# Kernel optimization log

Hardware: AMD Instinct MI355X
Metric: run time of the kernel (lower is better)

The kernel has to match this reference:

```python
import jax, jax.numpy as jnp
import numpy as np

BN_EPS = 1e-5


def conv2d(x, w, b, pad=1):
    # x: [B,Ci,H,W], w: [Co,Ci,kh,kw] (torch OIHW layout)
    y = jax.lax.conv_general_dilated(
        x, w, window_strides=(1, 1), padding=((pad, pad), (pad, pad)),
        dimension_numbers=("NCHW", "OIHW", "NCHW"))
    return y + b[None, :, None, None]


def conv_transpose2d(x, w, b):
    # torch ConvTranspose2d(k=3, stride=2, padding=1, output_padding=1)
    # w: [Ci, Co, 3, 3] (torch transpose-conv layout)
    # equivalent: lhs-dilated conv with flipped kernel, pad = (k-1-p, k-1-p+op) = (1, 2)
    wk = jnp.flip(w, axis=(2, 3)).transpose(1, 0, 2, 3)  # [Co, Ci, 3, 3]
    y = jax.lax.conv_general_dilated(
        x, wk, window_strides=(1, 1), padding=((1, 2), (1, 2)),
        lhs_dilation=(2, 2), dimension_numbers=("NCHW", "OIHW", "NCHW"))
    return y + b[None, :, None, None]


def setup_inputs() -> dict:
    key = jax.random.key(0)
    ks = jax.random.split(key, 10)
    B, Cin, Cout, E = 1024, 128, 64, 8
    s = lambda k, shape: jax.random.normal(k, shape, jnp.float32) * 0.05
    return {
        "x": jax.random.normal(ks[0], (B, Cin, 6, 6), jnp.float32),
        # gate params
        "gw": s(ks[1], (128, Cin, 3, 3)), "gb": jnp.zeros((128,), jnp.float32),
        "fc1_w": s(ks[2], (256, 128 * 9)), "fc1_b": jnp.zeros((256,), jnp.float32),
        "fc2_w": s(ks[3], (E, 256)), "fc2_b": jnp.zeros((E,), jnp.float32),
        # expert params, stacked over expert axis E (num_per_expert=1 block)
        "wd": s(ks[4], (E, Cin, Cout, 3, 3)), "bd": jnp.zeros((E, Cout), jnp.float32),
        "wc": s(ks[5], (E, Cout, Cout, 3, 3)), "bc": jnp.zeros((E, Cout), jnp.float32),
        # BatchNorm (inference / running stats)
        "bn_g": jnp.ones((E, Cout), jnp.float32),
        "bn_b": jnp.zeros((E, Cout), jnp.float32),
        "bn_m": s(ks[6], (E, Cout)),
        "bn_v": jax.random.uniform(ks[7], (E, Cout), jnp.float32, 0.5, 1.5),
        "top_k": 2,
    }


def reference(x, gw, gb, fc1_w, fc1_b, fc2_w, fc2_b,
              wd, bd, wc, bc, bn_g, bn_b, bn_m, bn_v, top_k):
    B = x.shape[0]

    # --- Gate: conv3x3 -> relu -> maxpool2x2 -> fc -> relu -> fc ---
    h = jax.nn.relu(conv2d(x, gw, gb))                       # [B,128,6,6]
    p = jax.lax.reduce_window(h, -jnp.inf, jax.lax.max,
                              (1, 1, 2, 2), (1, 1, 2, 2), "VALID")  # [B,128,3,3]
    z = jax.nn.relu(p.reshape(B, -1) @ fc1_w.T + fc1_b)
    logits = z @ fc2_w.T + fc2_b                             # [B,E]

    # --- All experts computed densely (as in source), vmapped over expert axis ---
    def expert(wd_e, bd_e, wc_e, bc_e, g_e, b_e, m_e, v_e):
        y = jax.nn.relu(conv_transpose2d(x, wd_e, bd_e))     # [B,Cout,12,12]
        y = conv2d(y, wc_e, bc_e)
        scale = (g_e * jax.lax.rsqrt(v_e + BN_EPS))[None, :, None, None]
        y = (y - m_e[None, :, None, None]) * scale + b_e[None, :, None, None]
        return jax.nn.relu(y)

    eo = jax.vmap(expert)(wd, bd, wc, bc, bn_g, bn_b, bn_m, bn_v)  # [E,B,C,12,12]

    # --- top-k routing: gather selected experts, softmax-weighted sum ---
    tw, ti = jax.lax.top_k(logits, top_k)                    # [B,k]
    tw = jax.nn.softmax(tw, axis=1)
    sel = jnp.take_along_axis(eo.transpose(1, 0, 2, 3, 4),
                              ti[:, :, None, None, None], axis=1)  # [B,k,C,12,12]
    return (sel * tw[:, :, None, None, None]).sum(axis=1)   # [B,C,12,12]
```

## Files before the change

### kernel.cpp

```cpp
#include <hip/hip_runtime.h>
#include <math.h>

typedef _Float16 f16x8 __attribute__((ext_vector_type(8)));
typedef float    f32x4 __attribute__((ext_vector_type(4)));

#define PWD_ELEMS 589824
#define PWC_ELEMS 294912
#define PWG_ELEMS 147456
#define PW1T_ELEMS 294912
#define WS_NEEDED_BYTES ((PWD_ELEMS + PWC_ELEMS + 2 * PWG_ELEMS) * 2 + 512 * 4 + 16384 + PW1T_ELEMS * 4)

__global__ void pack_weights(const float* __restrict__ wd,
                             const float* __restrict__ wc,
                             const float* __restrict__ gw,
                             const float* __restrict__ fc1_w,
                             const float* __restrict__ bc,
                             const float* __restrict__ bn_g,
                             const float* __restrict__ bn_b,
                             const float* __restrict__ bn_m,
                             const float* __restrict__ bn_v,
                             _Float16* __restrict__ pwd,
                             _Float16* __restrict__ pwc,
                             _Float16* __restrict__ pwg_hi,
                             _Float16* __restrict__ pwg_lo,
                             float* __restrict__ pbias,
                             float* __restrict__ pw1t)
{
  int i = blockIdx.x * 256 + threadIdx.x;
  if (i < PWD_ELEMS) {
    int j  = i & 7;
    int l  = (i >> 3) & 63;
    int nt = (i >> 9) & 3;
    int ks = (i >> 11) & 3;
    int rest = i >> 13;
    int t = rest % 9, e = rest / 9;
    int ky = t / 3, kx = t % 3;
    int k = ks * 32 + (l >> 4) * 8 + j;
    int n = nt * 16 + (l & 15);
    float v = wd[(((size_t)e * 128 + k) * 64 + n) * 9 + (2 - ky) * 3 + (2 - kx)];
    pwd[i] = (_Float16)v;
    return;
  }
  i -= PWD_ELEMS;
  if (i < PWC_ELEMS) {
    int j  = i & 7;
    int l  = (i >> 3) & 63;
    int nt = (i >> 9) & 3;
    int ks = (i >> 11) & 1;
    int rest = i >> 12;
    int t = rest % 9, e = rest / 9;
    int ky = t / 3, kx = t % 3;
    int k = ks * 32 + (l >> 4) * 8 + j;
    int n = nt * 16 + (l & 15);
    float scale = bn_g[e * 64 + n] * rsqrtf(bn_v[e * 64 + n] + 1e-5f);
    float v = wc[(((size_t)e * 64 + n) * 64 + k) * 9 + ky * 3 + kx] * scale;
    pwc[i] = (_Float16)v;
    return;
  }
  i -= PWC_ELEMS;
  if (i < PWG_ELEMS) {
    int j  = i & 7;
    int l  = (i >> 3) & 63;
    int nt = (i >> 9) & 7;
    int ks = (i >> 12) & 3;
    int t  = i >> 14;
    int ky = t / 3, kx = t % 3;
    int k = ks * 32 + (l >> 4) * 8 + j;
    int n = nt * 16 + (l & 15);
    float v = gw[(size_t)n * 1152 + k * 9 + ky * 3 + kx];
    _Float16 hi = (_Float16)v;
    pwg_hi[i] = hi;
    pwg_lo[i] = (_Float16)(v - (float)hi);
    return;
  }
  i -= PWG_ELEMS;
  if (i < 512) {
    int e = i >> 6, n = i & 63;
    float scale = bn_g[e * 64 + n] * rsqrtf(bn_v[e * 64 + n] + 1e-5f);
    pbias[i] = (bc[e * 64 + n] - bn_m[e * 64 + n]) * scale + bn_b[e * 64 + n];
    return;
  }
  i -= 512;
  if (i < PW1T_ELEMS) {
    int k = i >> 8, o = i & 255;
    pw1t[i] = fc1_w[(size_t)o * 1152 + k];
  }
}

__global__ __launch_bounds__(256, 4) void cmoe_gate(
    const float* __restrict__ x, const float* __restrict__ gb,
    const float* __restrict__ pw1t, const float* __restrict__ fc1_b,
    const float* __restrict__ fc2_w, const float* __restrict__ fc2_b,
    const _Float16* __restrict__ pwg_hi, const _Float16* __restrict__ pwg_lo,
    int* __restrict__ route_i, float* __restrict__ route_w)
{
  const int b = blockIdx.x;
  const int tid = threadIdx.x;

  __shared__ __align__(16) char smem[34816];
  _Float16* xg_hi = (_Float16*)smem;
  _Float16* xg_lo = (_Float16*)(smem + 17408);
  float* hbuf = (float*)smem;
  float* pbuf = (float*)(smem + 18432);
  float* zred = (float*)(smem + 23040);
  float* zbuf = (float*)(smem + 27136);
  float* slog = (float*)(smem + 28160);

  const int w    = tid >> 6;
  const int lane = tid & 63;
  const int lr   = lane & 15;
  const int lq   = lane >> 4;

  const float* xb = x + (size_t)b * 4608;
  for (int idx = tid; idx < 8192; idx += 256) {
    int sp = idx >> 7, ci = idx & 127;
    int row = sp >> 3, col = sp & 7;
    float v = 0.f;
    if (row >= 1 && row <= 6 && col >= 1 && col <= 6)
      v = xb[ci * 36 + (row - 1) * 6 + (col - 1)];
    _Float16 hi = (_Float16)v;
    xg_hi[sp * 136 + ci] = hi;
    xg_lo[sp * 136 + ci] = (_Float16)(v - (float)hi);
  }
  __syncthreads();

  {
    f32x4 Cg[3][2];
    {
      float b0 = gb[(2 * w) * 16 + lr];
      float b1 = gb[(2 * w + 1) * 16 + lr];
#pragma unroll
      for (int i = 0; i < 3; ++i) {
        Cg[i][0] = {b0, b0, b0, b0};
        Cg[i][1] = {b1, b1, b1, b1};
      }
    }
    int gA[3];
#pragma unroll
    for (int i = 0; i < 3; ++i) {
      int p = i * 16 + lr; if (p >= 36) p = 0;
      int oy = p / 6, ox = p % 6;
      gA[i] = (oy * 8 + ox) * 136 + lq * 8;
    }
    const _Float16* pgh = pwg_hi + lane * 8;
    const _Float16* pgl = pwg_lo + lane * 8;

    for (int t = 0; t < 9; ++t) {
      const int gtap = ((t / 3) * 8 + (t % 3)) * 136;
#pragma unroll
      for (int ks = 0; ks < 4; ++ks) {
        const int boff = ((t * 4 + ks) * 8 + 2 * w) * 512;
        f16x8 Bh0 = *(const f16x8*)(pgh + boff);
        f16x8 Bh1 = *(const f16x8*)(pgh + boff + 512);
        f16x8 Bl0 = *(const f16x8*)(pgl + boff);
        f16x8 Bl1 = *(const f16x8*)(pgl + boff + 512);
#pragma unroll
        for (int i = 0; i < 3; ++i) {
          f16x8 Ah = *(const f16x8*)(xg_hi + gA[i] + gtap + ks * 32);
          f16x8 Al = *(const f16x8*)(xg_lo + gA[i] + gtap + ks * 32);
          Cg[i][0] = __builtin_amdgcn_mfma_f32_16x16x32_f16(Ah, Bh0, Cg[i][0], 0, 0, 0);
          Cg[i][1] = __builtin_amdgcn_mfma_f32_16x16x32_f16(Ah, Bh1, Cg[i][1], 0, 0, 0);
          Cg[i][0] = __builtin_amdgcn_mfma_f32_16x16x32_f16(Al, Bh0, Cg[i][0], 0, 0, 0);
          Cg[i][1] = __builtin_amdgcn_mfma_f32_16x16x32_f16(Al, Bh1, Cg[i][1], 0, 0, 0);
          Cg[i][0] = __builtin_amdgcn_mfma_f32_16x16x32_f16(Ah, Bl0, Cg[i][0], 0, 0, 0);
          Cg[i][1] = __builtin_amdgcn_mfma_f32_16x16x32_f16(Ah, Bl1, Cg[i][1], 0, 0, 0);
        }
      }
    }
    __syncthreads();
#pragma unroll
    for (int i = 0; i < 3; ++i)
#pragma unroll
      for (int nn = 0; nn < 2; ++nn) {
        const int co_ = (2 * w + nn) * 16 + lr;
#pragma unroll
        for (int j = 0; j < 4; ++j) {
          int pix = i * 16 + lq * 4 + j;
          if (pix < 36) hbuf[co_ * 36 + pix] = fmaxf(Cg[i][nn][j], 0.f);
        }
      }
  }
  __syncthreads();

  for (int i = tid; i < 1152; i += 256) {
    int co_ = i / 9, r = i % 9, py = r / 3, px = r % 3;
    const float* hp = hbuf + co_ * 36 + (2 * py) * 6 + 2 * px;
    pbuf[i] = fmaxf(fmaxf(hp[0], hp[1]), fmaxf(hp[6], hp[7]));
  }
  __syncthreads();

  {
    const int g = lane;
    const float* pw = pw1t + w * 256 + 4 * g;
    f32x4 acc = {0.f, 0.f, 0.f, 0.f};
#pragma unroll 4
    for (int m = 0; m < 288; ++m) {
      float pv = pbuf[w + 4 * m];
      f32x4 wv = *(const f32x4*)(pw + m * 1024);
      acc.x += wv.x * pv; acc.y += wv.y * pv;
      acc.z += wv.z * pv; acc.w += wv.w * pv;
    }
    *(f32x4*)&zred[w * 256 + 4 * g] = acc;
  }
  __syncthreads();
  zbuf[tid] = fmaxf(zred[tid] + zred[256 + tid] + zred[512 + tid] + zred[768 + tid]
                    + fc1_b[tid], 0.f);
  __syncthreads();

  if (tid < 64) {
    int o = tid >> 3, t8 = tid & 7;
    float acc = 0.f;
    const float* wr = fc2_w + o * 256;
    for (int k = t8; k < 256; k += 8) acc += zbuf[k] * wr[k];
    acc += __shfl_xor(acc, 1);
    acc += __shfl_xor(acc, 2);
    acc += __shfl_xor(acc, 4);
    if (t8 == 0) slog[o] = acc + fc2_b[o];
  }
  __syncthreads();

  if (tid == 0) {
    int i0 = 0; float v0 = slog[0];
#pragma unroll
    for (int o = 1; o < 8; ++o) { float v = slog[o]; if (v > v0) { v0 = v; i0 = o; } }
    int i1 = (i0 == 0) ? 1 : 0; float v1 = slog[i1];
#pragma unroll
    for (int o = 0; o < 8; ++o) {
      if (o != i0) { float v = slog[o]; if (v > v1) { v1 = v; i1 = o; } }
    }
    float e1 = expf(v1 - v0);
    float inv = 1.f / (1.f + e1);
    route_i[2 * b] = i0; route_i[2 * b + 1] = i1;
    route_w[2 * b] = inv; route_w[2 * b + 1] = e1 * inv;
  }
}

#define ZOFF  4896
#define Y1OFF 5024

#define DECONV_TAP(KY, KX)                                                  \
  {                                                                         \
    constexpr int t_  = (KY) * 3 + (KX);                                    \
    constexpr int dy_ = ((KY) == 2) ? 1 : 0;                                \
    constexpr int dx_ = ((KX) == 2) ? 1 : 0;                                \
    int u0 = uA[0] + dy_, v0 = vA[0] + dx_;                                 \
    int u1 = uA[1] + dy_, v1 = vA[1] + dx_;                                 \
    int u2 = uA[2] + dy_, v2 = vA[2] + dx_;                                 \
    int b0_ = (pvA[0] && u0 < 6 && v0 < 6) ? (u0 * 6 + v0) * 136 : ZOFF;    \
    int b1_ = (pvA[1] && u1 < 6 && v1 < 6) ? (u1 * 6 + v1) * 136 : ZOFF;    \
    int b2_ = (pvA[2] && u2 < 6 && v2 < 6) ? (u2 * 6 + v2) * 136 : ZOFF;    \
    _Pragma("unroll")                                                       \
    for (int ks = 0; ks < 4; ++ks) {                                        \
      f16x8 Bf = *(const f16x8*)(pwd_e + (size_t)(t_ * 4 + ks) * 2048);     \
      f16x8 A0 = *(const f16x8*)(S + b0_ + lq * 8 + ks * 32);               \
      f16x8 A1 = *(const f16x8*)(S + b1_ + lq * 8 + ks * 32);               \
      f16x8 A2 = *(const f16x8*)(S + b2_ + lq * 8 + ks * 32);               \
      Cd0 = __builtin_amdgcn_mfma_f32_16x16x32_f16(A0, Bf, Cd0, 0, 0, 0);   \
      Cd1 = __builtin_amdgcn_mfma_f32_16x16x32_f16(A1, Bf, Cd1, 0, 0, 0);   \
      Cd2 = __builtin_amdgcn_mfma_f32_16x16x32_f16(A2, Bf, Cd2, 0, 0, 0);   \
    }                                                                       \
  }

#define STORE_CLASS(QY, QX)                                                 \
  _Pragma("unroll")                                                         \
  for (int i = 0; i < 3; ++i) {                                             \
    f32x4 Cv = (i == 0) ? Cd0 : ((i == 1) ? Cd1 : Cd2);                     \
    _Pragma("unroll")                                                       \
    for (int j = 0; j < 4; ++j) {                                           \
      int p = i * 16 + lq * 4 + j;                                          \
      if (p < 36) {                                                         \
        int u = p / 6, v = p - 6 * (p / 6);                                 \
        int oy = 2 * u + (QY), ox = 2 * v + (QX);                           \
        S[Y1OFF + ((oy + 1) * 14 + (ox + 1)) * 72 + co] =                   \
            (_Float16)fmaxf(Cv[j], 0.f);                                    \
      }                                                                     \
    }                                                                       \
  }

__global__ __launch_bounds__(256, 4) void cmoe_expert(
    const float* __restrict__ x,
    const float* __restrict__ bd,
    const _Float16* __restrict__ pwd, const _Float16* __restrict__ pwc,
    const float* __restrict__ pbias,
    const int* __restrict__ route_i, const float* __restrict__ route_w,
    float* __restrict__ out)
{
  const int b = blockIdx.x;
  const int tid = threadIdx.x;

  __shared__ __align__(16) char smem[38272];
  _Float16* S = (_Float16*)smem;
  float* sout = (float*)(smem + 10048);

  const int w    = tid >> 6;
  const int lane = tid & 63;
  const int lr   = lane & 15;
  const int lq   = lane >> 4;

  const int e0 = route_i[2 * b], e1 = route_i[2 * b + 1];
  const float w0 = route_w[2 * b], w1 = route_w[2 * b + 1];

  const float* xb = x + (size_t)b * 4608;
  for (int idx = tid; idx < 4608; idx += 256) {
    int ci = idx / 36, pix = idx - ci * 36;
    S[pix * 136 + ci] = (_Float16)xb[idx];
  }
  if (tid < 128) S[ZOFF + tid] = (_Float16)0.f;
  for (int idx = tid; idx < 52 * 72; idx += 256) {
    int sp = idx / 72, ci = idx % 72;
    int row, col;
    if (sp < 14)      { row = 0;       col = sp; }
    else if (sp < 28) { row = 13;      col = sp - 14; }
    else if (sp < 40) { row = sp - 27; col = 0; }
    else              { row = sp - 39; col = 13; }
    S[Y1OFF + (row * 14 + col) * 72 + ci] = (_Float16)0.f;
  }

  const int co = w * 16 + lr;

  int uA[3], vA[3], pvA[3];
#pragma unroll
  for (int i = 0; i < 3; ++i) {
    int p = i * 16 + lr;
    pvA[i] = (p < 36);
    int pc = pvA[i] ? p : 0;
    uA[i] = pc / 6; vA[i] = pc - 6 * (pc / 6);
  }
  int cA[9];
#pragma unroll
  for (int mt = 0; mt < 9; ++mt) {
    int pix = mt * 16 + lr;
    int oy = pix / 12, ox = pix - 12 * (pix / 12);
    cA[mt] = Y1OFF + (oy * 14 + ox) * 72 + lq * 8;
  }

  f32x4 facc[9];
#pragma unroll
  for (int mt = 0; mt < 9; ++mt) facc[mt] = {0.f, 0.f, 0.f, 0.f};

#pragma unroll 1
  for (int s = 0; s < 2; ++s) {
    const int e = s ? e1 : e0;
    const float wgt = s ? w1 : w0;
    const float db = bd[e * 64 + co];
    const _Float16* pwd_e = pwd + (size_t)e * (9 * 4 * 4 * 512) + w * 512 + lane * 8;

    __syncthreads();

    {
      f32x4 Cd0 = {db, db, db, db}, Cd1 = Cd0, Cd2 = Cd0;
      DECONV_TAP(0, 0) DECONV_TAP(0, 2) DECONV_TAP(2, 0) DECONV_TAP(2, 2)
      STORE_CLASS(1, 1)
    }
    {
      f32x4 Cd0 = {db, db, db, db}, Cd1 = Cd0, Cd2 = Cd0;
      DECONV_TAP(0, 1) DECONV_TAP(2, 1)
      STORE_CLASS(1, 0)
    }
    {
      f32x4 Cd0 = {db, db, db, db}, Cd1 = Cd0, Cd2 = Cd0;
      DECONV_TAP(1, 0) DECONV_TAP(1, 2)
      STORE_CLASS(0, 1)
    }
    {
      f32x4 Cd0 = {db, db, db, db}, Cd1 = Cd0, Cd2 = Cd0;
      DECONV_TAP(1, 1)
      STORE_CLASS(0, 0)
    }
    __syncthreads();

    f32x4 Cc[9];
    {
      const float cb = pbias[e * 64 + co];
#pragma unroll
      for (int mt = 0; mt < 9; ++mt) Cc[mt] = {cb, cb, cb, cb};
    }
    const _Float16* pwc_e = pwc + (size_t)e * (9 * 2 * 4 * 512) + w * 512 + lane * 8;

#pragma unroll
    for (int t = 0; t < 9; ++t) {
      const int ky = t / 3, kx = t % 3;
      const int aoff = (ky * 14 + kx) * 72;
#pragma unroll
      for (int ks = 0; ks < 2; ++ks) {
        f16x8 Bf = *(const f16x8*)(pwc_e + (size_t)(t * 2 + ks) * 2048);
#pragma unroll
        for (int mt = 0; mt < 9; ++mt) {
          f16x8 Af = *(const f16x8*)(S + cA[mt] + aoff + ks * 32);
          Cc[mt] = __builtin_amdgcn_mfma_f32_16x16x32_f16(Af, Bf, Cc[mt], 0, 0, 0);
        }
      }
    }

#pragma unroll
    for (int mt = 0; mt < 9; ++mt)
#pragma unroll
      for (int j = 0; j < 4; ++j)
        facc[mt][j] += wgt * fmaxf(Cc[mt][j], 0.f);
  }

  float* ob = out + (size_t)b * 9216;
  __syncthreads();
#pragma unroll
  for (int mt = 0; mt < 9; ++mt)
#pragma unroll
    for (int j = 0; j < 4; ++j) {
      int pix = mt * 16 + lq * 4 + j;
      if (pix < 72) sout[pix * 65 + co] = facc[mt][j];
    }
  __syncthreads();
  for (int j2 = tid; j2 < 4608; j2 += 256) {
    int c2 = j2 / 72, px = j2 - 72 * c2;
    ob[c2 * 144 + px] = sout[px * 65 + c2];
  }
  __syncthreads();
#pragma unroll
  for (int mt = 0; mt < 9; ++mt)
#pragma unroll
    for (int j = 0; j < 4; ++j) {
      int pix = mt * 16 + lq * 4 + j;
      if (pix >= 72) sout[(pix - 72) * 65 + co] = facc[mt][j];
    }
  __syncthreads();
  for (int j2 = tid; j2 < 4608; j2 += 256) {
    int c2 = j2 / 72, px = j2 - 72 * c2;
    ob[c2 * 144 + 72 + px] = sout[px * 65 + c2];
  }
}


#define DECONV_TAPS(q, ky, r)                                              \
  _Pragma("unroll")                                                        \
  for (int ox = 0; ox < 12; ++ox) {                                        \
    _Pragma("unroll")                                                      \
    for (int kx = 0; kx < 3; ++kx) {                                       \
      const int ss = ox + kx - 1;                                          \
      if (ss >= 0 && ss <= 10 && (ss & 1) == 0)                            \
        dacc[q][ox] += xr[r][ss >> 1] * w9[8 - ((ky) * 3 + (kx))];         \
    }                                                                      \
  }

__global__ __launch_bounds__(256, 2) void cmoe_ref(
    const float* __restrict__ x,
    const float* __restrict__ gw, const float* __restrict__ gb,
    const float* __restrict__ fc1_w, const float* __restrict__ fc1_b,
    const float* __restrict__ fc2_w, const float* __restrict__ fc2_b,
    const float* __restrict__ wd, const float* __restrict__ bd,
    const float* __restrict__ wc, const float* __restrict__ bc,
    const float* __restrict__ bn_g, const float* __restrict__ bn_b,
    const float* __restrict__ bn_m, const float* __restrict__ bn_v,
    float* __restrict__ out)
{
  const int b = blockIdx.x;
  const int tid = threadIdx.x;

  __shared__ float sx[128 * 48];
  __shared__ float sbuf[64 * 168];
  __shared__ int   se[2];
  __shared__ float swv[2];

  const float* xb = x + (size_t)b * 4608;
  for (int i = tid; i < 4608; i += 256) {
    int ci = i / 36, rem = i % 36;
    sx[ci * 48 + 6 + rem] = xb[i];
  }
  for (int i = tid; i < 128 * 12; i += 256) {
    int ci = i / 12, j = i % 12;
    sx[ci * 48 + (j < 6 ? j : 36 + j)] = 0.f;
  }
  __syncthreads();

  {
    const int co = tid >> 1;
    const int hh = tid & 1;
    float hacc[3][6];
    const float bias = gb[co];
#pragma unroll
    for (int q = 0; q < 3; ++q)
#pragma unroll
      for (int ox = 0; ox < 6; ++ox) hacc[q][ox] = bias;

    const float* wbase = gw + co * 1152;
    const float* xsb = sx + hh * 18;
    for (int ci = 0; ci < 128; ++ci) {
      const float* wr = wbase + ci * 9;
      float w9[9];
#pragma unroll
      for (int k = 0; k < 9; ++k) w9[k] = wr[k];
      const float* xr = xsb + ci * 48;
#pragma unroll
      for (int s = 0; s < 5; ++s) {
        float r8[8];
        r8[0] = 0.f; r8[7] = 0.f;
#pragma unroll
        for (int c = 0; c < 6; ++c) r8[c + 1] = xr[s * 6 + c];
#pragma unroll
        for (int ky = 0; ky < 3; ++ky) {
          const int q = s - ky;
          if (q >= 0 && q < 3) {
#pragma unroll
            for (int ox = 0; ox < 6; ++ox)
#pragma unroll
              for (int kx = 0; kx < 3; ++kx)
                hacc[q][ox] += r8[ox + kx] * w9[ky * 3 + kx];
          }
        }
      }
    }
#pragma unroll
    for (int q = 0; q < 3; ++q)
#pragma unroll
      for (int ox = 0; ox < 6; ++ox)
        sbuf[co * 36 + (3 * hh + q) * 6 + ox] = fmaxf(hacc[q][ox], 0.f);
  }
  __syncthreads();

  {
    float* sp = sbuf + 4608;
    for (int i = tid; i < 1152; i += 256) {
      int co = i / 9, r = i % 9, py = r / 3, px = r % 3;
      const float* hp = sbuf + co * 36 + (2 * py) * 6 + 2 * px;
      sp[i] = fmaxf(fmaxf(hp[0], hp[1]), fmaxf(hp[6], hp[7]));
    }
  }
  __syncthreads();

  {
    const float* sp = sbuf + 4608;
    float* sz = sbuf + 5760;
    float acc = fc1_b[tid];
    const float4* wr = (const float4*)(fc1_w + (size_t)tid * 1152);
    const float4* p4 = (const float4*)sp;
#pragma unroll 4
    for (int k = 0; k < 288; ++k) {
      float4 wv4 = wr[k], pv = p4[k];
      acc += wv4.x * pv.x + wv4.y * pv.y + wv4.z * pv.z + wv4.w * pv.w;
    }
    sz[tid] = fmaxf(acc, 0.f);
  }
  __syncthreads();

  {
    const float* sz = sbuf + 5760;
    float* slog = sbuf + 6016;
    if (tid < 8) {
      float acc = fc2_b[tid];
      const float* wr = fc2_w + tid * 256;
      for (int k = 0; k < 256; ++k) acc += sz[k] * wr[k];
      slog[tid] = acc;
    }
  }
  __syncthreads();

  if (tid == 0) {
    const float* slog = sbuf + 6016;
    int i0 = 0; float v0 = slog[0];
#pragma unroll
    for (int o = 1; o < 8; ++o) { float v = slog[o]; if (v > v0) { v0 = v; i0 = o; } }
    int i1 = (i0 == 0) ? 1 : 0; float v1 = slog[i1];
#pragma unroll
    for (int o = 0; o < 8; ++o) {
      if (o != i0) { float v = slog[o]; if (v > v1) { v1 = v; i1 = o; } }
    }
    float e1 = expf(v1 - v0);
    float inv = 1.f / (1.f + e1);
    se[0] = i0; se[1] = i1; swv[0] = inv; swv[1] = e1 * inv;
  }
  __syncthreads();

  for (int i = tid; i < 64 * 24; i += 256) {
    int ci = i / 24, j = i % 24;
    sbuf[ci * 168 + (j < 12 ? j : 144 + j)] = 0.f;
  }

  const int wv = tid >> 6;
  const int co = tid & 63;
  const int iyb = (wv & 1) ? (3 * wv - 1) / 2 : (3 * wv) / 2;

  float facc[3][12];
#pragma unroll
  for (int q = 0; q < 3; ++q)
#pragma unroll
    for (int ox = 0; ox < 12; ++ox) facc[q][ox] = 0.f;

  for (int slot = 0; slot < 2; ++slot) {
    const int e = se[slot];
    const float wgt = swv[slot];

    float dacc[3][12];
    {
      const float db = bd[e * 64 + co];
#pragma unroll
      for (int q = 0; q < 3; ++q)
#pragma unroll
        for (int ox = 0; ox < 12; ++ox) dacc[q][ox] = db;

      const float* wdb = wd + ((size_t)e * 128 * 64 + co) * 9;
      for (int ci = 0; ci < 128; ++ci) {
        const float* wr = wdb + (size_t)ci * 576;
        float w9[9];
#pragma unroll
        for (int k = 0; k < 9; ++k) w9[k] = wr[k];
        float xr[3][6];
#pragma unroll
        for (int r = 0; r < 3; ++r)
#pragma unroll
          for (int c = 0; c < 6; ++c)
            xr[r][c] = sx[ci * 48 + (iyb + r + 1) * 6 + c];
        if (wv & 1) {
          DECONV_TAPS(0, 0, 0)
          DECONV_TAPS(0, 2, 1)
          DECONV_TAPS(1, 1, 1)
          DECONV_TAPS(2, 0, 1)
          DECONV_TAPS(2, 2, 2)
        } else {
          DECONV_TAPS(0, 1, 0)
          DECONV_TAPS(1, 0, 0)
          DECONV_TAPS(1, 2, 1)
          DECONV_TAPS(2, 1, 1)
        }
      }
    }

    __syncthreads();
#pragma unroll
    for (int q = 0; q < 3; ++q)
#pragma unroll
      for (int ox = 0; ox < 12; ++ox)
        sbuf[co * 168 + (3 * wv + q + 1) * 12 + ox] = fmaxf(dacc[q][ox], 0.f);
    __syncthreads();

    float cacc[3][12];
    const float cb = bc[e * 64 + co];
#pragma unroll
    for (int q = 0; q < 3; ++q)
#pragma unroll
      for (int ox = 0; ox < 12; ++ox) cacc[q][ox] = cb;

    const float* wcb = wc + ((size_t)e * 64 + co) * 576;
    for (int ci = 0; ci < 64; ++ci) {
      const float* wr = wcb + ci * 9;
      float w9[9];
#pragma unroll
      for (int k = 0; k < 9; ++k) w9[k] = wr[k];
#pragma unroll
      for (int s = 0; s < 5; ++s) {
        float r14[14];
        r14[0] = 0.f; r14[13] = 0.f;
#pragma unroll
        for (int c = 0; c < 12; ++c) r14[c + 1] = sbuf[ci * 168 + (3 * wv + s) * 12 + c];
#pragma unroll
        for (int ky = 0; ky < 3; ++ky) {
          const int q = s - ky;
          if (q >= 0 && q < 3) {
#pragma unroll
            for (int ox = 0; ox < 12; ++ox)
#pragma unroll
              for (int kx = 0; kx < 3; ++kx)
                cacc[q][ox] += r14[ox + kx] * w9[ky * 3 + kx];
          }
        }
      }
    }

    const float g = bn_g[e * 64 + co], bb = bn_b[e * 64 + co];
    const float mm = bn_m[e * 64 + co], vvv = bn_v[e * 64 + co];
    const float scale = g * rsqrtf(vvv + 1e-5f);
#pragma unroll
    for (int q = 0; q < 3; ++q)
#pragma unroll
      for (int ox = 0; ox < 12; ++ox) {
        float v = (cacc[q][ox] - mm) * scale + bb;
        facc[q][ox] += wgt * fmaxf(v, 0.f);
      }
  }

  float* ob = out + ((size_t)b * 64 + co) * 144;
#pragma unroll
  for (int q = 0; q < 3; ++q)
#pragma unroll
    for (int ox = 0; ox < 12; ++ox)
      ob[(3 * wv + q) * 12 + ox] = facc[q][ox];
}

extern "C" void kernel_launch(void* const* d_in, const int* in_sizes, int n_in,
                              void* d_out, int out_size, void* d_ws, size_t ws_size,
                              hipStream_t stream) {
  const float* x     = (const float*)d_in[0];
  const float* gw    = (const float*)d_in[1];
  const float* gb    = (const float*)d_in[2];
  const float* fc1_w = (const float*)d_in[3];
  const float* fc1_b = (const float*)d_in[4];
  const float* fc2_w = (const float*)d_in[5];
  const float* fc2_b = (const float*)d_in[6];
  const float* wd    = (const float*)d_in[7];
  const float* bd    = (const float*)d_in[8];
  const float* wc    = (const float*)d_in[9];
  const float* bc    = (const float*)d_in[10];
  const float* bn_g  = (const float*)d_in[11];
  const float* bn_b  = (const float*)d_in[12];
  const float* bn_m  = (const float*)d_in[13];
  const float* bn_v  = (const float*)d_in[14];
  float* out = (float*)d_out;

  if (ws_size >= (size_t)WS_NEEDED_BYTES && d_ws != nullptr) {
    _Float16* pwd    = (_Float16*)d_ws;
    _Float16* pwc    = pwd + PWD_ELEMS;
    _Float16* pwg_hi = pwc + PWC_ELEMS;
    _Float16* pwg_lo = pwg_hi + PWG_ELEMS;
    float*    pbias  = (float*)(pwg_lo + PWG_ELEMS);
    int*      route_i = (int*)(pbias + 512);
    float*    route_w = (float*)(route_i + 2048);
    float*    pw1t   = route_w + 2048;

    int total = PWD_ELEMS + PWC_ELEMS + PWG_ELEMS + 512 + PW1T_ELEMS;
    pack_weights<<<dim3((total + 255) / 256), dim3(256), 0, stream>>>(
        wd, wc, gw, fc1_w, bc, bn_g, bn_b, bn_m, bn_v,
        pwd, pwc, pwg_hi, pwg_lo, pbias, pw1t);
    cmoe_gate<<<dim3(1024), dim3(256), 0, stream>>>(
        x, gb, pw1t, fc1_b, fc2_w, fc2_b, pwg_hi, pwg_lo, route_i, route_w);
    cmoe_expert<<<dim3(1024), dim3(256), 0, stream>>>(
        x, bd, pwd, pwc, pbias, route_i, route_w, out);
  } else {
    cmoe_ref<<<dim3(1024), dim3(256), 0, stream>>>(
        x, gw, gb, fc1_w, fc1_b, fc2_w, fc2_b,
        wd, bd, wc, bc, bn_g, bn_b, bn_m, bn_v, out);
  }
}
```

Before: 170.7 us.

## Process two samples per gate block to reuse conv and fc1 weight loads

The gate kernel now handles two batch samples per workgroup: it stages both inputs in shared memory, reuses each loaded gate-conv weight fragment for MFMAs on both samples, and reuses each fc1 weight vector for two dot products. The grid is halved and shared memory roughly doubles, with launch bounds relaxed to 2 blocks per CU. This targets the global/L2 weight traffic of the gate, at the cost of lower occupancy and fewer blocks in flight.

```diff
diff --git a/kernel.cpp b/kernel.cpp
--- a/kernel.cpp
+++ b/kernel.cpp
@@ -87,60 +87,61 @@
   }
 }
 
-__global__ __launch_bounds__(256, 4) void cmoe_gate(
+__global__ __launch_bounds__(256, 2) void cmoe_gate(
     const float* __restrict__ x, const float* __restrict__ gb,
     const float* __restrict__ pw1t, const float* __restrict__ fc1_b,
     const float* __restrict__ fc2_w, const float* __restrict__ fc2_b,
     const _Float16* __restrict__ pwg_hi, const _Float16* __restrict__ pwg_lo,
     int* __restrict__ route_i, float* __restrict__ route_w)
 {
-  const int b = blockIdx.x;
+  const int b2 = blockIdx.x;
   const int tid = threadIdx.x;
 
-  __shared__ __align__(16) char smem[34816];
+  __shared__ __align__(16) char smem[72256];
   _Float16* xg_hi = (_Float16*)smem;
-  _Float16* xg_lo = (_Float16*)(smem + 17408);
-  float* hbuf = (float*)smem;
-  float* pbuf = (float*)(smem + 18432);
-  float* zred = (float*)(smem + 23040);
-  float* zbuf = (float*)(smem + 27136);
-  float* slog = (float*)(smem + 28160);
+  _Float16* xg_lo = (_Float16*)(smem + 34816);
+  float* zred = (float*)(smem + 44032);
+  float* slog = (float*)(smem + 54272);
 
   const int w    = tid >> 6;
   const int lane = tid & 63;
   const int lr   = lane & 15;
   const int lq   = lane >> 4;
 
-  const float* xb = x + (size_t)b * 4608;
-  for (int idx = tid; idx < 8192; idx += 256) {
-    int sp = idx >> 7, ci = idx & 127;
+  for (int idx = tid; idx < 2 * 8192; idx += 256) {
+    int s  = idx >> 13;
+    int r  = idx & 8191;
+    int sp = r >> 7, ci = r & 127;
     int row = sp >> 3, col = sp & 7;
     float v = 0.f;
     if (row >= 1 && row <= 6 && col >= 1 && col <= 6)
-      v = xb[ci * 36 + (row - 1) * 6 + (col - 1)];
+      v = x[(size_t)(2 * b2 + s) * 4608 + ci * 36 + (row - 1) * 6 + (col - 1)];
     _Float16 hi = (_Float16)v;
-    xg_hi[sp * 136 + ci] = hi;
-    xg_lo[sp * 136 + ci] = (_Float16)(v - (float)hi);
-  }
-  __syncthreads();
+    xg_hi[s * 8704 + sp * 136 + ci] = hi;
+    xg_lo[s * 8704 + sp * 136 + ci] = (_Float16)(v - (float)hi);
+  }
+  __syncthreads();
+
+  int gA[3];
+#pragma unroll
+  for (int i = 0; i < 3; ++i) {
+    int p = i * 16 + lr; if (p >= 36) p = 0;
+    int oy = p / 6, ox = p % 6;
+    gA[i] = (oy * 8 + ox) * 136 + lq * 8;
+  }
 
   {
-    f32x4 Cg[3][2];
+    f32x4 Cg[2][3][2];
     {
       float b0 = gb[(2 * w) * 16 + lr];
       float b1 = gb[(2 * w + 1) * 16 + lr];
 #pragma unroll
-      for (int i = 0; i < 3; ++i) {
-        Cg[i][0] = {b0, b0, b0, b0};
-        Cg[i][1] = {b1, b1, b1, b1};
-      }
-    }
-    int gA[3];
-#pragma unroll
-    for (int i = 0; i < 3; ++i) {
-      int p = i * 16 + lr; if (p >= 36) p = 0;
-      int oy = p / 6, ox = p % 6;
-      gA[i] = (oy * 8 + ox) * 136 + lq * 8;
+      for (int s = 0; s < 2; ++s)
+#pragma unroll
+        for (int i = 0; i < 3; ++i) {
+          Cg[s][i][0] = {b0, b0, b0, b0};
+          Cg[s][i][1] = {b1, b1, b1, b1};
+        }
     }
     const _Float16* pgh = pwg_hi + lane * 8;
     const _Float16* pgl = pwg_lo + lane * 8;
@@ -155,83 +156,124 @@
         f16x8 Bl0 = *(const f16x8*)(pgl + boff);
         f16x8 Bl1 = *(const f16x8*)(pgl + boff + 512);
 #pragma unroll
-        for (int i = 0; i < 3; ++i) {
-          f16x8 Ah = *(const f16x8*)(xg_hi + gA[i] + gtap + ks * 32);
-          f16x8 Al = *(const f16x8*)(xg_lo + gA[i] + gtap + ks * 32);
-          Cg[i][0] = __builtin_amdgcn_mfma_f32_16x16x32_f16(Ah, Bh0, Cg[i][0], 0, 0, 0);
-          Cg[i][1] = __builtin_amdgcn_mfma_f32_16x16x32_f16(Ah, Bh1, Cg[i][1], 0, 0, 0);
-          Cg[i][0] = __builtin_amdgcn_mfma_f32_16x16x32_f16(Al, Bh0, Cg[i][0], 0, 0, 0);
-          Cg[i][1] = __builtin_amdgcn_mfma_f32_16x16x32_f16(Al, Bh1, Cg[i][1], 0, 0, 0);
-          Cg[i][0] = __builtin_amdgcn_mfma_f32_16x16x32_f16(Ah, Bl0, Cg[i][0], 0, 0, 0);
-          Cg[i][1] = __builtin_amdgcn_mfma_f32_16x16x32_f16(Ah, Bl1, Cg[i][1], 0, 0, 0);
+        for (int s = 0; s < 2; ++s)
+#pragma unroll
+          for (int i = 0; i < 3; ++i) {
+            f16x8 Ah = *(const f16x8*)(xg_hi + s * 8704 + gA[i] + gtap + ks * 32);
+            f16x8 Al = *(const f16x8*)(xg_lo + s * 8704 + gA[i] + gtap + ks * 32);
+            Cg[s][i][0] = __builtin_amdgcn_mfma_f32_16x16x32_f16(Ah, Bh0, Cg[s][i][0], 0, 0, 0);
+            Cg[s][i][1] = __builtin_amdgcn_mfma_f32_16x16x32_f16(Ah, Bh1, Cg[s][i][1], 0, 0, 0);
+            Cg[s][i][0] = __builtin_amdgcn_mfma_f32_16x16x32_f16(Al, Bh0, Cg[s][i][0], 0, 0, 0);
+            Cg[s][i][1] = __builtin_amdgcn_mfma_f32_16x16x32_f16(Al, Bh1, Cg[s][i][1], 0, 0, 0);
+            Cg[s][i][0] = __builtin_amdgcn_mfma_f32_16x16x32_f16(Ah, Bl0, Cg[s][i][0], 0, 0, 0);
+            Cg[s][i][1] = __builtin_amdgcn_mfma_f32_16x16x32_f16(Ah, Bl1, Cg[s][i][1], 0, 0, 0);
+          }
+      }
+    }
+    __syncthreads();
+#pragma unroll
+    for (int s = 0; s < 2; ++s) {
+      float* hb = (float*)(smem + 34816 + s * 18432);
+#pragma unroll
+      for (int i = 0; i < 3; ++i)
+#pragma unroll
+        for (int nn = 0; nn < 2; ++nn) {
+          const int co_ = (2 * w + nn) * 16 + lr;
+#pragma unroll
+          for (int j = 0; j < 4; ++j) {
+            int pix = i * 16 + lq * 4 + j;
+            if (pix < 36) hb[co_ * 36 + pix] = fmaxf(Cg[s][i][nn][j], 0.f);
+          }
         }
+    }
+  }
+  __syncthreads();
+
+  {
+    float pr[2][5];
+#pragma unroll
+    for (int r = 0; r < 5; ++r) {
+      int i = tid + 256 * r;
+      if (i < 1152) {
+        int co_ = i / 9, q = i % 9, py = q / 3, px = q % 3;
+#pragma unroll
+        for (int s = 0; s < 2; ++s) {
+          const float* hp = (const float*)(smem + 34816 + s * 18432)
+                            + co_ * 36 + (2 * py) * 6 + 2 * px;
+          pr[s][r] = fmaxf(fmaxf(hp[0], hp[1]), fmaxf(hp[6], hp[7]));
+        }
       }
     }
     __syncthreads();
 #pragma unroll
-    for (int i = 0; i < 3; ++i)
-#pragma unroll
-      for (int nn = 0; nn < 2; ++nn) {
-        const int co_ = (2 * w + nn) * 16 + lr;
-#pragma unroll
-        for (int j = 0; j < 4; ++j) {
-          int pix = i * 16 + lq * 4 + j;
-          if (pix < 36) hbuf[co_ * 36 + pix] = fmaxf(Cg[i][nn][j], 0.f);
-        }
-      }
-  }
-  __syncthreads();
-
-  for (int i = tid; i < 1152; i += 256) {
-    int co_ = i / 9, r = i % 9, py = r / 3, px = r % 3;
-    const float* hp = hbuf + co_ * 36 + (2 * py) * 6 + 2 * px;
-    pbuf[i] = fmaxf(fmaxf(hp[0], hp[1]), fmaxf(hp[6], hp[7]));
+    for (int r = 0; r < 5; ++r) {
+      int i = tid + 256 * r;
+      if (i < 1152) {
+        ((float*)(smem + 34816))[i] = pr[0][r];
+        ((float*)(smem + 39424))[i] = pr[1][r];
+      }
+    }
   }
   __syncthreads();
 
   {
-    const int g = lane;
-    const float* pw = pw1t + w * 256 + 4 * g;
-    f32x4 acc = {0.f, 0.f, 0.f, 0.f};
+    const float* pw = pw1t + w * 256 + 4 * lane;
+    const float* p0 = (const float*)(smem + 34816);
+    const float* p1 = (const float*)(smem + 39424);
+    f32x4 a0 = {0.f, 0.f, 0.f, 0.f}, a1 = {0.f, 0.f, 0.f, 0.f};
 #pragma unroll 4
     for (int m = 0; m < 288; ++m) {
-      float pv = pbuf[w + 4 * m];
+      float pv0 = p0[w + 4 * m];
+      float pv1 = p1[w + 4 * m];
       f32x4 wv = *(const f32x4*)(pw + m * 1024);
-      acc.x += wv.x * pv; acc.y += wv.y * pv;
-      acc.z += wv.z * pv; acc.w += wv.w * pv;
-    }
-    *(f32x4*)&zred[w * 256 + 4 * g] = acc;
-  }
-  __syncthreads();
-  zbuf[tid] = fmaxf(zred[tid] + zred[256 + tid] + zred[512 + tid] + zred[768 + tid]
-                    + fc1_b[tid], 0.f);
-  __syncthreads();
-
-  if (tid < 64) {
-    int o = tid >> 3, t8 = tid & 7;
+      a0.x += wv.x * pv0; a0.y += wv.y * pv0; a0.z += wv.z * pv0; a0.w += wv.w * pv0;
+      a1.x += wv.x * pv1; a1.y += wv.y * pv1; a1.z += wv.z * pv1; a1.w += wv.w * pv1;
+    }
+    *(f32x4*)&zred[(0 * 4 + w) * 256 + 4 * lane] = a0;
+    *(f32x4*)&zred[(1 * 4 + w) * 256 + 4 * lane] = a1;
+  }
+  __syncthreads();
+  float* z0 = (float*)(smem + 52224);
+  float* z1 = (float*)(smem + 53248);
+  {
+    float fb = fc1_b[tid];
+    z0[tid] = fmaxf(zred[tid] + zred[256 + tid] + zred[512 + tid] + zred[768 + tid] + fb, 0.f);
+    z1[tid] = fmaxf(zred[1024 + tid] + zred[1280 + tid] + zred[1536 + tid] + zred[1792 + tid] + fb, 0.f);
+  }
+  __syncthreads();
+
+  if (tid < 128) {
+    int s = tid >> 6, l = tid & 63;
+    int o = l >> 3, t8 = l & 7;
+    const float* zz = s ? z1 : z0;
+    const float* wr = fc2_w + o * 256;
     float acc = 0.f;
-    const float* wr = fc2_w + o * 256;
-    for (int k = t8; k < 256; k += 8) acc += zbuf[k] * wr[k];
+    for (int k = t8; k < 256; k += 8) acc += zz[k] * wr[k];
     acc += __shfl_xor(acc, 1);
     acc += __shfl_xor(acc, 2);
     acc += __shfl_xor(acc, 4);
-    if (t8 == 0) slog[o] = acc + fc2_b[o];
+    if (t8 == 0) slog[s * 8 + o] = acc + fc2_b[o];
   }
   __syncthreads();
 
   if (tid == 0) {
-    int i0 = 0; float v0 = slog[0];
-#pragma unroll
-    for (int o = 1; o < 8; ++o) { float v = slog[o]; if (v > v0) { v0 = v; i0 = o; } }
-    int i1 = (i0 == 0) ? 1 : 0; float v1 = slog[i1];
-#pragma unroll
-    for (int o = 0; o < 8; ++o) {
-      if (o != i0) { float v = slog[o]; if (v > v1) { v1 = v; i1 = o; } }
-    }
-    float e1 = expf(v1 - v0);
-    float inv = 1.f / (1.f + e1);
-    route_i[2 * b] = i0; route_i[2 * b + 1] = i1;
-    route_w[2 * b] = inv; route_w[2 * b + 1] = e1 * inv;
+#pragma unroll
+    for (int s = 0; s < 2; ++s) {
+      const float* sl = slog + s * 8;
+      int i0 = 0; float v0 = sl[0];
+#pragma unroll
+      for (int o = 1; o < 8; ++o) { float v = sl[o]; if (v > v0) { v0 = v; i0 = o; } }
+      int i1 = (i0 == 0) ? 1 : 0; float v1 = sl[i1];
+#pragma unroll
+      for (int o = 0; o < 8; ++o) {
+        if (o != i0) { float v = sl[o]; if (v > v1) { v1 = v; i1 = o; } }
+      }
+      float e1 = expf(v1 - v0);
+      float inv = 1.f / (1.f + e1);
+      int sb = 2 * b2 + s;
+      route_i[2 * sb] = i0; route_i[2 * sb + 1] = i1;
+      route_w[2 * sb] = inv; route_w[2 * sb + 1] = e1 * inv;
+    }
   }
 }
 
@@ -717,7 +759,7 @@
     pack_weights<<<dim3((total + 255) / 256), dim3(256), 0, stream>>>(
         wd, wc, gw, fc1_w, bc, bn_g, bn_b, bn_m, bn_v,
         pwd, pwc, pwg_hi, pwg_lo, pbias, pw1t);
-    cmoe_gate<<<dim3(1024), dim3(256), 0, stream>>>(
+    cmoe_gate<<<dim3(512), dim3(256), 0, stream>>>(
         x, gb, pw1t, fc1_b, fc2_w, fc2_b, pwg_hi, pwg_lo, route_i, route_w);
     cmoe_expert<<<dim3(1024), dim3(256), 0, stream>>>(
         x, bd, pwd, pwc, pbias, route_i, route_w, out);
```

Result: faster. 158.0 us (-7.4%).
